# Optimization experiments

Measured on AMD Instinct MI355X. Metric: run time of the kernel, lower is better.

The kernel has to match this reference:

```python
import jax, jax.numpy as jnp
import numpy as np

B, N, L = 2, 2048, 2048
DQ, DKV, H, WF = 1024, 1024, 16, 4
HD = DQ // H
EPS = 1e-5


def _ln(x, g, b):
    m = jnp.mean(x, axis=-1, keepdims=True)
    v = jnp.mean(jnp.square(x - m), axis=-1, keepdims=True)
    return (x - m) * jax.lax.rsqrt(v + EPS) * g + b


def setup_inputs() -> dict:
    key = jax.random.key(0)
    ks = jax.random.split(key, 12)
    s = 0.02
    return {
        "x_q": jax.random.normal(ks[0], (B, N, DQ), jnp.float32),
        "x_kv": jax.random.normal(ks[1], (B, L, DKV), jnp.float32),
        "qn_g": jnp.ones((DQ,), jnp.float32),
        "qn_b": jnp.zeros((DQ,), jnp.float32),
        "kvn_g": jnp.ones((DKV,), jnp.float32),
        "kvn_b": jnp.zeros((DKV,), jnp.float32),
        "Wq": jax.random.normal(ks[2], (DQ, DQ), jnp.float32) * s,
        "bq": jnp.zeros((DQ,), jnp.float32),
        "Wk": jax.random.normal(ks[3], (DQ, DKV), jnp.float32) * s,
        "bk": jnp.zeros((DQ,), jnp.float32),
        "Wv": jax.random.normal(ks[4], (DQ, DKV), jnp.float32) * s,
        "bv": jnp.zeros((DQ,), jnp.float32),
        "Wo": jax.random.normal(ks[5], (DQ, DQ), jnp.float32) * s,
        "bo": jnp.zeros((DQ,), jnp.float32),
        "n2_g": jnp.ones((DQ,), jnp.float32),
        "n2_b": jnp.zeros((DQ,), jnp.float32),
        "W1": jax.random.normal(ks[6], (WF * DQ, DQ), jnp.float32) * s,
        "b1": jnp.zeros((WF * DQ,), jnp.float32),
        "W2": jax.random.normal(ks[7], (DQ, WF * DQ), jnp.float32) * s,
        "b2": jnp.zeros((DQ,), jnp.float32),
    }


def reference(x_q, x_kv, qn_g, qn_b, kvn_g, kvn_b, Wq, bq, Wk, bk, Wv, bv,
              Wo, bo, n2_g, n2_b, W1, b1, W2, b2):
    # projections (torch Linear: x @ W.T + b)
    q = (_ln(x_q, qn_g, qn_b) @ Wq.T + bq).reshape(B, N, H, HD)
    kvn = _ln(x_kv, kvn_g, kvn_b)
    k = (kvn @ Wk.T + bk).reshape(B, L, H, HD)
    v = (kvn @ Wv.T + bv).reshape(B, L, H, HD)

    # attention with softmax-1: exp(s)/(1 + sum exp(s)), numerically stable
    scale = 1.0 / jnp.sqrt(jnp.float32(HD))
    s = jnp.einsum("bnhd,blhd->bhnl", q, k) * scale  # [B,H,N,L]
    m = jnp.max(s, axis=-1, keepdims=True)
    m = jnp.maximum(m, 0.0)  # include the implicit zero logit of softmax-1
    p = jnp.exp(s - m)
    denom = jnp.sum(p, axis=-1, keepdims=True) + jnp.exp(-m)
    attn = p / denom
    attn_out = jnp.einsum("bhnl,blhd->bnhd", attn, v).reshape(B, N, DQ)

    # residual + out proj
    x = x_q + (attn_out @ Wo.T + bo)
    # residual MLP (GELU, exact/erf as torch nn.GELU default)
    h = jax.nn.gelu(_ln(x, n2_g, n2_b) @ W1.T + b1, approximate=False)
    x = x + (h @ W2.T + b2)
    return x
```

## Files before the change

### kernel.cpp

```cpp
#include <hip/hip_runtime.h>
#include <hip/hip_bf16.h>
#include <stdint.h>

#define DEV __device__ __forceinline__

typedef unsigned short ushort_t;
typedef __attribute__((ext_vector_type(8))) short bf16x8;
typedef __attribute__((ext_vector_type(4))) float f32x4;

DEV uint32_t f2bf2(float lo, float hi) {
  uint32_t d;
  asm("v_cvt_pk_bf16_f32 %0, %1, %2" : "=v"(d) : "v"(lo), "v"(hi));
  return d;
}
DEV ushort_t f2bf(float f) { return (ushort_t)f2bf2(f, f); }

DEV void gload_lds16(const void* gp, void* lp) {
  __builtin_amdgcn_global_load_lds(
      (__attribute__((address_space(1))) void*)(void*)(uintptr_t)gp,
      (__attribute__((address_space(3))) void*)lp, 16, 0, 0);
}

DEV float gelu_fast(float x) {
  const float z = fabsf(x) * 0.70710678118654752f;
  const float t = __builtin_amdgcn_rcpf(fmaf(0.3275911f, z, 1.0f));
  float p = fmaf(1.061405429f, t, -1.453152027f);
  p = fmaf(p, t, 1.421413741f);
  p = fmaf(p, t, -0.284496736f);
  p = fmaf(p, t, 0.254829592f);
  p *= t;
  const float e = __builtin_amdgcn_exp2f(z * z * -1.4426950408889634f);
  const float er = fmaf(-p, e, 1.0f);
  const float s = copysignf(er, x);
  return 0.5f * x * (1.0f + s);
}

DEV void ln_row(const float* __restrict__ x, const float* __restrict__ g,
                const float* __restrict__ be, ushort_t* __restrict__ out, int row) {
  const int t = threadIdx.x;
  const float4 v = ((const float4*)(x + (size_t)row * 1024))[t];
  float s = v.x + v.y + v.z + v.w;
  float sq = v.x * v.x + v.y * v.y + v.z * v.z + v.w * v.w;
#pragma unroll
  for (int d = 1; d < 64; d <<= 1) { s += __shfl_xor(s, d); sq += __shfl_xor(sq, d); }
  __shared__ float sm[8];
  const int w = t >> 6, lane = t & 63;
  if (lane == 0) { sm[w * 2] = s; sm[w * 2 + 1] = sq; }
  __syncthreads();
  s = sm[0] + sm[2] + sm[4] + sm[6];
  sq = sm[1] + sm[3] + sm[5] + sm[7];
  const float mean = s * (1.f / 1024.f);
  const float var = sq * (1.f / 1024.f) - mean * mean;
  const float rstd = rsqrtf(var + 1e-5f);
  const float4 gv = ((const float4*)g)[t];
  const float4 bv = ((const float4*)be)[t];
  uint2 o;
  o.x = f2bf2((v.x - mean) * rstd * gv.x + bv.x, (v.y - mean) * rstd * gv.y + bv.y);
  o.y = f2bf2((v.z - mean) * rstd * gv.z + bv.z, (v.w - mean) * rstd * gv.w + bv.w);
  ((uint2*)(out + (size_t)row * 1024))[t] = o;
}

__global__ __launch_bounds__(256) void cvt_ln(
    const float* __restrict__ Wq, const float* __restrict__ Wk,
    const float* __restrict__ Wv, const float* __restrict__ Wo,
    const float* __restrict__ W1, const float* __restrict__ W2,
    ushort_t* __restrict__ WQKVB, ushort_t* __restrict__ WoB,
    ushort_t* __restrict__ W1B, ushort_t* __restrict__ W2B,
    const float* __restrict__ x_q, const float* __restrict__ x_kv,
    const float* __restrict__ qg, const float* __restrict__ qb,
    const float* __restrict__ kg, const float* __restrict__ kb,
    ushort_t* __restrict__ oq, ushort_t* __restrict__ okv) {
  if (blockIdx.x < 12288) {
    int i = blockIdx.x * 256 + threadIdx.x;
    const float* src; ushort_t* dst; int j;
    if (i < 262144)            { src = Wq; dst = WQKVB;            j = i; }
    else if (i < 524288)       { src = Wk; dst = WQKVB + 1048576;  j = i - 262144; }
    else if (i < 786432)       { src = Wv; dst = WQKVB + 2097152;  j = i - 524288; }
    else if (i < 1048576)      { src = Wo; dst = WoB;              j = i - 786432; }
    else if (i < 2097152)      { src = W1; dst = W1B;              j = i - 1048576; }
    else                       { src = W2; dst = W2B;              j = i - 2097152; }
    float4 v = ((const float4*)src)[j];
    uint2 o; o.x = f2bf2(v.x, v.y); o.y = f2bf2(v.z, v.w);
    ((uint2*)dst)[j] = o;
  } else {
    const int r = blockIdx.x - 12288;
    if (r < 4096) ln_row(x_q, qg, qb, oq, r);
    else ln_row(x_kv, kg, kb, okv, r - 4096);
  }
}

__global__ __launch_bounds__(256) void ln_bf16(const float* __restrict__ x,
                                               const float* __restrict__ g,
                                               const float* __restrict__ be,
                                               ushort_t* __restrict__ out) {
  ln_row(x, g, be, out, blockIdx.x);
}

DEV void xcd_remap(int gx, int gy, int& bx, int& by) {
  const int lin = by * gx + bx;
  const int xcd = lin & 7, s = lin >> 3;
  by = xcd * (gy >> 3) + s / gx;
  bx = s % gx;
}

enum { EPI_BF16 = 0, EPI_KV = 1, EPI_RESID = 2, EPI_GELU = 3, EPI_QKV = 4 };

template <int BM, int TN, int BK, int EPI>
__global__ __launch_bounds__(256, (BM == 64) ? 4 : 3) void gemm_bt(
    const ushort_t* __restrict__ A,
    const ushort_t* __restrict__ A2,
    const ushort_t* __restrict__ Wb,
    const float* __restrict__ bias, const float* __restrict__ bias2,
    const float* __restrict__ bias3,
    const float* __restrict__ resid,
    void* __restrict__ outp, void* __restrict__ outp2, void* __restrict__ outp3,
    int M, int N, int K, float oscale) {
  constexpr int WAVES_N = (TN == 128 || BM == 64) ? 2 : 1;
  constexpr int WAVES_M = 4 / WAVES_N;
  constexpr int NI = BM / WAVES_M / 16;
  constexpr int NJ = TN / WAVES_N / 16;
  constexpr int CH = BK / 8;
  constexpr int NA = (BM * CH) / 256;
  constexpr int NBL = (TN * CH) / 256;
  constexpr int KS = BK / 32;
  __shared__ ushort_t As[2][BM * BK];
  __shared__ ushort_t Bs[2][TN * BK];
  const int t = threadIdx.x;
  const int w = t >> 6, lane = t & 63;
  const int qd = lane >> 4, ql = lane & 15;
  int bx = blockIdx.x, by = blockIdx.y;
  xcd_remap(gridDim.x, gridDim.y, bx, by);
  const int m0 = by * BM, n0 = bx * TN;
  const int wm = (w / WAVES_N) * (BM / WAVES_M);
  const int wn = (w % WAVES_N) * (TN / WAVES_N);
  const int sw = (BK == 64) ? (ql & 7) : ((ql >> 1) & 3);

  const ushort_t* Ause = (EPI == EPI_QKV && n0 >= 1024) ? A2 : A;

  const ushort_t* pa[NA];
#pragma unroll
  for (int p = 0; p < NA; p++) {
    int n = p * 256 + t, row = n / CH, c = n % CH;
    int g = (BK == 64) ? (c ^ (row & 7)) : (c ^ ((row >> 1) & 3));
    pa[p] = Ause + (size_t)(m0 + row) * K + g * 8;
  }
  const ushort_t* pb[NBL];
#pragma unroll
  for (int p = 0; p < NBL; p++) {
    int n = p * 256 + t, row = n / CH, c = n % CH;
    int g = (BK == 64) ? (c ^ (row & 7)) : (c ^ ((row >> 1) & 3));
    pb[p] = Wb + (size_t)(n0 + row) * K + g * 8;
  }

#pragma unroll
  for (int p = 0; p < NA; p++) { gload_lds16(pa[p], &As[0][(p * 256 + t) * 8]); pa[p] += BK; }
#pragma unroll
  for (int p = 0; p < NBL; p++) { gload_lds16(pb[p], &Bs[0][(p * 256 + t) * 8]); pb[p] += BK; }
  __syncthreads();

  f32x4 acc[NI][NJ] = {};
  const int NIT = K / BK;
  int cur = 0;

  for (int it = 0; it < NIT; ++it) {
    if (it + 1 < NIT) {
#pragma unroll
      for (int p = 0; p < NA; p++) { gload_lds16(pa[p], &As[1 ^ cur][(p * 256 + t) * 8]); pa[p] += BK; }
#pragma unroll
      for (int p = 0; p < NBL; p++) { gload_lds16(pb[p], &Bs[1 ^ cur][(p * 256 + t) * 8]); pb[p] += BK; }
    }
    const ushort_t* Ac = As[cur];
    const ushort_t* Bc = Bs[cur];
#pragma unroll
    for (int ks = 0; ks < KS; ks++) {
      bf16x8 af[NI], bf[NJ];
#pragma unroll
      for (int i = 0; i < NI; i++)
        af[i] = *(const bf16x8*)&Ac[(wm + i * 16 + ql) * BK + ((ks * 4 + qd) ^ sw) * 8];
#pragma unroll
      for (int j = 0; j < NJ; j++)
        bf[j] = *(const bf16x8*)&Bc[(wn + j * 16 + ql) * BK + ((ks * 4 + qd) ^ sw) * 8];
#pragma unroll
      for (int i = 0; i < NI; i++)
#pragma unroll
        for (int j = 0; j < NJ; j++)
          acc[i][j] = __builtin_amdgcn_mfma_f32_16x16x32_bf16(af[i], bf[j], acc[i][j], 0, 0, 0);
    }
    __syncthreads();
    cur ^= 1;
  }

#pragma unroll
  for (int i = 0; i < NI; i++) {
    const int mr = m0 + wm + i * 16 + qd * 4;
#pragma unroll
    for (int j = 0; j < NJ; j++) {
      const int col = n0 + wn + j * 16 + ql;
      f32x4 v = acc[i][j];
      if constexpr (EPI == EPI_BF16) {
        const float bb = bias[col];
        ushort_t* o = (ushort_t*)outp;
#pragma unroll
        for (int r = 0; r < 4; r++) o[(size_t)(mr + r) * N + col] = f2bf((v[r] + bb) * oscale);
      } else if constexpr (EPI == EPI_QKV) {
        if (col < 1024) {
          const float bb = bias[col];
          ushort_t* o = (ushort_t*)outp;
#pragma unroll
          for (int r = 0; r < 4; r++) o[(size_t)(mr + r) * 1024 + col] = f2bf((v[r] + bb) * oscale);
        } else if (col < 2048) {
          const int c2 = col - 1024;
          const float bb = bias2[c2];
          ushort_t* o = (ushort_t*)outp2;
#pragma unroll
          for (int r = 0; r < 4; r++) o[(size_t)(mr + r) * 1024 + c2] = f2bf(v[r] + bb);
        } else {
          const int vc = col - 2048;
          const float bb = bias3[vc];
          const int h = vc >> 6, d = vc & 63;
          const int b = mr >> 11, l0 = mr & 2047;
          uint2 pk;
          pk.x = f2bf2(v[0] + bb, v[1] + bb);
          pk.y = f2bf2(v[2] + bb, v[3] + bb);
          *(uint2*)((ushort_t*)outp3 + ((((size_t)b * 16 + h) * 64 + d) * 2048 + l0)) = pk;
        }
      } else if constexpr (EPI == EPI_RESID) {
        const float bb = bias[col];
        float* o = (float*)outp;
#pragma unroll
        for (int r = 0; r < 4; r++) {
          size_t idx = (size_t)(mr + r) * N + col;
          o[idx] = resid[idx] + v[r] + bb;
        }
      } else if constexpr (EPI == EPI_GELU) {
        const float bb = bias[col];
        ushort_t* o = (ushort_t*)outp;
#pragma unroll
        for (int r = 0; r < 4; r++)
          o[(size_t)(mr + r) * N + col] = f2bf(gelu_fast(v[r] + bb));
      }
    }
  }
}

template <int EPI>
__global__ __launch_bounds__(512, 2) void gemm256v2(
    const ushort_t* __restrict__ A, const ushort_t* __restrict__ Wb,
    const float* __restrict__ bias,
    void* __restrict__ outp, int M, int N, int K, float oscale) {
  __shared__ ushort_t As[2][256 * 64];
  __shared__ ushort_t Bs[2][256 * 64];
  const int t = threadIdx.x;
  const int w = t >> 6, lane = t & 63;
  const int qd = lane >> 4, ql = lane & 15;
  const int wr = w >> 2, wc = w & 3;
  int bx = blockIdx.x, by = blockIdx.y;
  xcd_remap(gridDim.x, gridDim.y, bx, by);
  const int m0 = by * 256, n0 = bx * 256;
  const int sw = ql & 7;

  const ushort_t* pa[4];
  const ushort_t* pb[4];
#pragma unroll
  for (int p = 0; p < 4; p++) {
    const int n = p * 512 + t, row = n >> 3, c = (n & 7) ^ (row & 7);
    pa[p] = A + (size_t)(m0 + row) * K + c * 8;
    pb[p] = Wb + (size_t)(n0 + row) * K + c * 8;
  }

#pragma unroll
  for (int p = 0; p < 4; p++) { gload_lds16(pa[p], &As[0][(p * 512 + t) * 8]); pa[p] += 64; }
#pragma unroll
  for (int p = 0; p < 4; p++) { gload_lds16(pb[p], &Bs[0][(p * 512 + t) * 8]); pb[p] += 64; }
  __syncthreads();

  f32x4 acc[8][4] = {};
  const int NT = K / 64;
  int cur = 0;

#define AFREAD(KS)                                                              \
  _Pragma("unroll") for (int i = 0; i < 8; i++)                                 \
      af[i] = *(const bf16x8*)&Ac[(wr * 128 + i * 16 + ql) * 64 +               \
                                  (((KS) * 4 + qd) ^ sw) * 8];
#define BFREAD(KS, NH)                                                          \
  _Pragma("unroll") for (int jj = 0; jj < 2; jj++)                              \
      bf[jj] = *(const bf16x8*)&Bc[(wc * 64 + (NH) * 32 + jj * 16 + ql) * 64 +  \
                                   (((KS) * 4 + qd) ^ sw) * 8];
#define MM(NH)                                                                  \
  __builtin_amdgcn_s_setprio(1);                                                \
  _Pragma("unroll") for (int i = 0; i < 8; i++)                                 \
      _Pragma("unroll") for (int jj = 0; jj < 2; jj++)                          \
          acc[i][(NH) * 2 + jj] = __builtin_amdgcn_mfma_f32_16x16x32_bf16(      \
              af[i], bf[jj], acc[i][(NH) * 2 + jj], 0, 0, 0);                   \
  __builtin_amdgcn_s_setprio(0);

  for (int T = 0; T < NT; ++T) {
    const ushort_t* Ac = As[cur];
    const ushort_t* Bc = Bs[cur];
    ushort_t* An = As[cur ^ 1];
    ushort_t* Bn = Bs[cur ^ 1];
    const bool st = (T + 1 < NT);
    bf16x8 af[8], bf[2];

    if (st) {
#pragma unroll
      for (int p = 0; p < 4; p++) { gload_lds16(pa[p], &An[(p * 512 + t) * 8]); pa[p] += 64; }
#pragma unroll
      for (int p = 0; p < 4; p++) { gload_lds16(pb[p], &Bn[(p * 512 + t) * 8]); pb[p] += 64; }
    }
    AFREAD(0)
    BFREAD(0, 0)
    MM(0)
    __builtin_amdgcn_s_barrier();

    BFREAD(0, 1)
    MM(1)
    __builtin_amdgcn_s_barrier();

    AFREAD(1)
    BFREAD(1, 0)
    MM(0)
    __builtin_amdgcn_s_barrier();

    BFREAD(1, 1)
    MM(1)
    if (st) asm volatile("s_waitcnt vmcnt(0)" ::: "memory");
    __builtin_amdgcn_sched_barrier(0);
    __builtin_amdgcn_s_barrier();
    __builtin_amdgcn_sched_barrier(0);
    cur ^= 1;
  }
#undef AFREAD
#undef BFREAD
#undef MM

#pragma unroll
  for (int i = 0; i < 8; i++) {
    const int mr = m0 + wr * 128 + i * 16 + qd * 4;
#pragma unroll
    for (int j = 0; j < 4; j++) {
      const int col = n0 + wc * 64 + j * 16 + ql;
      f32x4 v = acc[i][j];
      if constexpr (EPI == EPI_GELU) {
        const float bb = bias[col];
        ushort_t* o = (ushort_t*)outp;
#pragma unroll
        for (int r = 0; r < 4; r++)
          o[(size_t)(mr + r) * N + col] = f2bf(gelu_fast(v[r] + bb));
      } else if constexpr (EPI == EPI_BF16) {
        const float bb = bias[col];
        ushort_t* o = (ushort_t*)outp;
#pragma unroll
        for (int r = 0; r < 4; r++)
          o[(size_t)(mr + r) * N + col] = f2bf((v[r] + bb) * oscale);
      }
    }
  }
}

__global__ __launch_bounds__(256, 2) void flash_attn(const ushort_t* __restrict__ Qg,
                                                     const ushort_t* __restrict__ Kg,
                                                     const ushort_t* __restrict__ VTg,
                                                     ushort_t* __restrict__ Og) {
  __shared__ ushort_t QPs[128 * 64];
  __shared__ ushort_t Ks[2][64 * 64];
  __shared__ ushort_t Vs[2][64 * 64];
  const int t = threadIdx.x, w = t >> 6, lane = t & 63;
  const int qd = lane >> 4, ql = lane & 15;
  int bx = blockIdx.x, bh = blockIdx.y;
  xcd_remap(gridDim.x, gridDim.y, bx, bh);
  const int b = bh >> 4, h = bh & 15;
  const int n0 = bx * 128;
  const ushort_t* Qp = Qg + ((size_t)b * 2048 + n0) * 1024 + h * 64;
  const ushort_t* Kp = Kg + (size_t)b * 2048 * 1024 + h * 64;
  const ushort_t* Vp = VTg + (size_t)bh * 64 * 2048;
  const int sw = ql & 7;

  const ushort_t* kp2[2];
  const ushort_t* vp2[2];
#pragma unroll
  for (int p = 0; p < 2; p++) {
    int n = p * 256 + t, row = n >> 3, c = (n & 7) ^ (row & 7);
    kp2[p] = Kp + (size_t)row * 1024 + c * 8;
    vp2[p] = Vp + (size_t)row * 2048 + c * 8;
  }

#pragma unroll
  for (int p = 0; p < 4; p++) {
    int n = p * 256 + t, row = n >> 3, c = (n & 7) ^ (row & 7);
    gload_lds16(Qp + (size_t)row * 1024 + c * 8, &QPs[n * 8]);
  }
#pragma unroll
  for (int p = 0; p < 2; p++) { gload_lds16(kp2[p], &Ks[0][(p * 256 + t) * 8]); kp2[p] += 64 * 1024; }
  __syncthreads();

  bf16x8 aq[2][2];
#pragma unroll
  for (int i = 0; i < 2; i++)
#pragma unroll
    for (int ks = 0; ks < 2; ks++)
      aq[i][ks] = *(const bf16x8*)&QPs[(w * 32 + i * 16 + ql) * 64 + ((ks * 4 + qd) ^ sw) * 8];
  __syncthreads();

  f32x4 accA[4][2], accB[4][2];
  f32x4 accO[2][4] = {};
  float lro2[2] = {0.f, 0.f};
  const f32x4 ZZ = {0.f, 0.f, 0.f, 0.f};

#define QKSTEP(ACC, KSLOT)                                                                \
  { const ushort_t* Kc_ = &Ks[KSLOT][0];                                                  \
    bf16x8 bk[4];                                                                         \
    _Pragma("unroll") for (int j = 0; j < 4; j++)                                         \
      bk[j] = *(const bf16x8*)&Kc_[(j * 16 + ql) * 64 + ((0 + qd) ^ sw) * 8];             \
    __builtin_amdgcn_s_setprio(1);                                                        \
    _Pragma("unroll") for (int j = 0; j < 4; j++)                                         \
      _Pragma("unroll") for (int i = 0; i < 2; i++)                                       \
        ACC[j][i] = __builtin_amdgcn_mfma_f32_16x16x32_bf16(bk[j], aq[i][0], ZZ, 0, 0, 0);\
    __builtin_amdgcn_s_setprio(0);                                                        \
    _Pragma("unroll") for (int j = 0; j < 4; j++)                                         \
      bk[j] = *(const bf16x8*)&Kc_[(j * 16 + ql) * 64 + ((4 + qd) ^ sw) * 8];             \
    __builtin_amdgcn_s_setprio(1);                                                        \
    _Pragma("unroll") for (int j = 0; j < 4; j++)                                         \
      _Pragma("unroll") for (int i = 0; i < 2; i++)                                       \
        ACC[j][i] = __builtin_amdgcn_mfma_f32_16x16x32_bf16(bk[j], aq[i][1], ACC[j][i], 0, 0, 0); \
    __builtin_amdgcn_s_setprio(0);                                                        \
  }

#define SMSTEP(ACC)                                                                       \
  _Pragma("unroll") for (int j = 0; j < 4; j++)                                           \
    _Pragma("unroll") for (int i = 0; i < 2; i++) {                                       \
      f32x4 pp;                                                                           \
      _Pragma("unroll") for (int r = 0; r < 4; r++) {                                     \
        pp[r] = __builtin_amdgcn_exp2f(ACC[j][i][r]);                                     \
        lro2[i] += pp[r];                                                                 \
      }                                                                                   \
      const int nn = w * 32 + i * 16 + ql;                                                \
      const int coff = (((j * 2 + (qd >> 1)) ^ sw) << 3) + ((qd & 1) << 2);               \
      uint2 pk_; pk_.x = f2bf2(pp[0], pp[1]); pk_.y = f2bf2(pp[2], pp[3]);                \
      *(uint2*)&QPs[nn * 64 + coff] = pk_;                                                \
    }

#define PVSTEP(VSLOT)                                                                     \
  { const ushort_t* Vc_ = &Vs[VSLOT][0];                                                  \
    _Pragma("unroll") for (int ks = 0; ks < 2; ks++) {                                    \
      bf16x8 ap[2], bv[4];                                                                \
      _Pragma("unroll") for (int i = 0; i < 2; i++)                                       \
        ap[i] = *(const bf16x8*)&QPs[(w * 32 + i * 16 + ql) * 64 + ((ks * 4 + qd) ^ sw) * 8]; \
      _Pragma("unroll") for (int jo = 0; jo < 4; jo++)                                    \
        bv[jo] = *(const bf16x8*)&Vc_[(jo * 16 + ql) * 64 + ((ks * 4 + qd) ^ sw) * 8];    \
      __builtin_amdgcn_s_setprio(1);                                                      \
      _Pragma("unroll") for (int i = 0; i < 2; i++)                                       \
        _Pragma("unroll") for (int jo = 0; jo < 4; jo++)                                  \
          accO[i][jo] = __builtin_amdgcn_mfma_f32_16x16x32_bf16(ap[i], bv[jo], accO[i][jo], 0, 0, 0); \
      __builtin_amdgcn_s_setprio(0);                                                      \
    }                                                                                     \
  }

#define STAGE_K(SLOT)                                                                     \
  _Pragma("unroll") for (int q_ = 0; q_ < 2; q_++) {                                      \
    gload_lds16(kp2[q_], &Ks[SLOT][(q_ * 256 + t) * 8]); kp2[q_] += 64 * 1024;            \
  }
#define STAGE_V(SLOT)                                                                     \
  _Pragma("unroll") for (int q_ = 0; q_ < 2; q_++) {                                      \
    gload_lds16(vp2[q_], &Vs[SLOT][(q_ * 256 + t) * 8]); vp2[q_] += 64;                   \
  }

  STAGE_K(1)
  STAGE_V(0)
  QKSTEP(accA, 0)
  __syncthreads();

  for (int tt = 1; tt < 31; tt += 2) {
    STAGE_K(0)
    STAGE_V(1)
    QKSTEP(accB, 1)
    SMSTEP(accA)
    PVSTEP(0)
    __syncthreads();
    STAGE_K(1)
    STAGE_V(0)
    QKSTEP(accA, 0)
    SMSTEP(accB)
    PVSTEP(1)
    __syncthreads();
  }
  STAGE_V(1)
  QKSTEP(accB, 1)
  SMSTEP(accA)
  PVSTEP(0)
  __syncthreads();
  SMSTEP(accB)
  PVSTEP(1)

#undef QKSTEP
#undef SMSTEP
#undef PVSTEP
#undef STAGE_K
#undef STAGE_V

  float dn[2];
#pragma unroll
  for (int i = 0; i < 2; i++) {
    float l = lro2[i];
    l += __shfl_xor(l, 16);
    l += __shfl_xor(l, 32);
    dn[i] = l + 1.0f;
  }

#pragma unroll
  for (int i = 0; i < 2; i++)
#pragma unroll
    for (int r = 0; r < 4; r++) {
      const float inv = 1.0f / __shfl(dn[i], qd * 4 + r);
      const int row = n0 + w * 32 + i * 16 + qd * 4 + r;
#pragma unroll
      for (int jo = 0; jo < 4; jo++)
        Og[((size_t)b * 2048 + row) * 1024 + h * 64 + jo * 16 + ql] =
            f2bf(accO[i][jo][r] * inv);
    }
}

extern "C" void kernel_launch(void* const* d_in, const int* in_sizes, int n_in,
                              void* d_out, int out_size, void* d_ws, size_t ws_size,
                              hipStream_t stream) {
  const float* x_q = (const float*)d_in[0];
  const float* x_kv = (const float*)d_in[1];
  const float* qn_g = (const float*)d_in[2];
  const float* qn_b = (const float*)d_in[3];
  const float* kvn_g = (const float*)d_in[4];
  const float* kvn_b = (const float*)d_in[5];
  const float* Wq = (const float*)d_in[6];
  const float* bq = (const float*)d_in[7];
  const float* Wk = (const float*)d_in[8];
  const float* bk = (const float*)d_in[9];
  const float* Wv = (const float*)d_in[10];
  const float* bv = (const float*)d_in[11];
  const float* Wo = (const float*)d_in[12];
  const float* bo = (const float*)d_in[13];
  const float* n2_g = (const float*)d_in[14];
  const float* n2_b = (const float*)d_in[15];
  const float* W1 = (const float*)d_in[16];
  const float* b1 = (const float*)d_in[17];
  const float* W2 = (const float*)d_in[18];
  const float* b2 = (const float*)d_in[19];

  char* ws = (char*)d_ws;
  const size_t MB = 1ull << 20;
  ushort_t* WQKVB = (ushort_t*)(ws + 0 * MB);
  ushort_t* WoB = (ushort_t*)(ws + 6 * MB);
  ushort_t* W1B = (ushort_t*)(ws + 8 * MB);
  ushort_t* W2B = (ushort_t*)(ws + 16 * MB);
  ushort_t* LNQ = (ushort_t*)(ws + 24 * MB);
  ushort_t* LNKV = (ushort_t*)(ws + 32 * MB);
  ushort_t* Qb = (ushort_t*)(ws + 40 * MB);
  ushort_t* Kb = (ushort_t*)(ws + 48 * MB);
  ushort_t* VTb = (ushort_t*)(ws + 56 * MB);
  ushort_t* AOb = (ushort_t*)(ws + 64 * MB);
  float* Xf = (float*)(ws + 72 * MB);
  ushort_t* LN2 = (ushort_t*)(ws + 88 * MB);
  ushort_t* Hb = (ushort_t*)(ws + 24 * MB);

  const float QSCALE = 0.18033688011112042f;

  cvt_ln<<<20480, 256, 0, stream>>>(Wq, Wk, Wv, Wo, W1, W2, WQKVB, WoB, W1B, W2B,
                                    x_q, x_kv, qn_g, qn_b, kvn_g, kvn_b, LNQ, LNKV);

  gemm_bt<128, 128, 32, EPI_QKV><<<dim3(24, 32), 256, 0, stream>>>(
      LNQ, LNKV, WQKVB, bq, bk, bv, nullptr, Qb, Kb, VTb, 4096, 3072, 1024, QSCALE);

  flash_attn<<<dim3(16, 32), 256, 0, stream>>>(Qb, Kb, VTb, AOb);

  gemm_bt<64, 64, 64, EPI_RESID><<<dim3(16, 64), 256, 0, stream>>>(
      AOb, nullptr, WoB, bo, nullptr, nullptr, x_q, Xf, nullptr, nullptr,
      4096, 1024, 1024, 1.0f);
  ln_bf16<<<4096, 256, 0, stream>>>(Xf, n2_g, n2_b, LN2);
  gemm256v2<EPI_GELU><<<dim3(16, 16), 512, 0, stream>>>(
      LN2, W1B, b1, Hb, 4096, 4096, 1024, 1.0f);
  gemm_bt<64, 64, 64, EPI_RESID><<<dim3(16, 64), 256, 0, stream>>>(
      Hb, nullptr, W2B, b2, nullptr, nullptr, Xf, (float*)d_out, nullptr, nullptr,
      4096, 1024, 4096, 1.0f);
}
```

Measured before the change: 350.9 us.

## Overlap Wo/W1/W2 bf16 conversion with QKV GEMM via extra grid z-slice

Moves the fp32-to-bf16 conversion of Wo, W1 and W2 out of the initial cvt_ln kernel and into a second z-slice of the QKV GEMM launch. Those extra blocks only convert weights and return, so the memory-bound conversion can run alongside the compute-bound GEMM instead of before it. This shortens the serial prologue. The extra blocks compete with the GEMM for CUs and bandwidth, and the template now carries hardcoded grid constants (24, 196608).

After: 349.9 us. About the same (-0.3%).

```diff
diff --git a/kernel.cpp b/kernel.cpp
--- a/kernel.cpp
+++ b/kernel.cpp
@@ -62,28 +62,22 @@
 
 __global__ __launch_bounds__(256) void cvt_ln(
     const float* __restrict__ Wq, const float* __restrict__ Wk,
-    const float* __restrict__ Wv, const float* __restrict__ Wo,
-    const float* __restrict__ W1, const float* __restrict__ W2,
-    ushort_t* __restrict__ WQKVB, ushort_t* __restrict__ WoB,
-    ushort_t* __restrict__ W1B, ushort_t* __restrict__ W2B,
+    const float* __restrict__ Wv, ushort_t* __restrict__ WQKVB,
     const float* __restrict__ x_q, const float* __restrict__ x_kv,
     const float* __restrict__ qg, const float* __restrict__ qb,
     const float* __restrict__ kg, const float* __restrict__ kb,
     ushort_t* __restrict__ oq, ushort_t* __restrict__ okv) {
-  if (blockIdx.x < 12288) {
+  if (blockIdx.x < 3072) {
     int i = blockIdx.x * 256 + threadIdx.x;
-    const float* src; ushort_t* dst; int j;
-    if (i < 262144)            { src = Wq; dst = WQKVB;            j = i; }
-    else if (i < 524288)       { src = Wk; dst = WQKVB + 1048576;  j = i - 262144; }
-    else if (i < 786432)       { src = Wv; dst = WQKVB + 2097152;  j = i - 524288; }
-    else if (i < 1048576)      { src = Wo; dst = WoB;              j = i - 786432; }
-    else if (i < 2097152)      { src = W1; dst = W1B;              j = i - 1048576; }
-    else                       { src = W2; dst = W2B;              j = i - 2097152; }
+    const float* src; int j;
+    if (i < 262144)      { src = Wq; j = i; }
+    else if (i < 524288) { src = Wk; j = i - 262144; }
+    else                 { src = Wv; j = i - 524288; }
     float4 v = ((const float4*)src)[j];
     uint2 o; o.x = f2bf2(v.x, v.y); o.y = f2bf2(v.z, v.w);
-    ((uint2*)dst)[j] = o;
+    ((uint2*)WQKVB)[i] = o;
   } else {
-    const int r = blockIdx.x - 12288;
+    const int r = blockIdx.x - 3072;
     if (r < 4096) ln_row(x_q, qg, qb, oq, r);
     else ln_row(x_kv, kg, kb, okv, r - 4096);
   }
@@ -114,7 +108,27 @@
     const float* __restrict__ bias3,
     const float* __restrict__ resid,
     void* __restrict__ outp, void* __restrict__ outp2, void* __restrict__ outp3,
-    int M, int N, int K, float oscale) {
+    int M, int N, int K, float oscale,
+    const float* __restrict__ cWo = nullptr, const float* __restrict__ cW1 = nullptr,
+    const float* __restrict__ cW2 = nullptr, ushort_t* __restrict__ dWoB = nullptr,
+    ushort_t* __restrict__ dW1B = nullptr, ushort_t* __restrict__ dW2B = nullptr) {
+  if constexpr (EPI == EPI_QKV) {
+    if (blockIdx.z != 0) {
+      const int id0 = (blockIdx.y * 24 + blockIdx.x) * 256 + threadIdx.x;
+#pragma unroll
+      for (int it = 0; it < 12; it++) {
+        const int u = id0 + it * 196608;
+        const float* src; ushort_t* dst; int j;
+        if (u < 262144)       { src = cWo; dst = dWoB; j = u; }
+        else if (u < 1310720) { src = cW1; dst = dW1B; j = u - 262144; }
+        else                  { src = cW2; dst = dW2B; j = u - 1310720; }
+        float4 v = ((const float4*)src)[j];
+        uint2 o; o.x = f2bf2(v.x, v.y); o.y = f2bf2(v.z, v.w);
+        ((uint2*)dst)[j] = o;
+      }
+      return;
+    }
+  }
   constexpr int WAVES_N = (TN == 128 || BM == 64) ? 2 : 1;
   constexpr int WAVES_M = 4 / WAVES_N;
   constexpr int NI = BM / WAVES_M / 16;
@@ -562,11 +576,12 @@
 
   const float QSCALE = 0.18033688011112042f;
 
-  cvt_ln<<<20480, 256, 0, stream>>>(Wq, Wk, Wv, Wo, W1, W2, WQKVB, WoB, W1B, W2B,
+  cvt_ln<<<11264, 256, 0, stream>>>(Wq, Wk, Wv, WQKVB,
                                     x_q, x_kv, qn_g, qn_b, kvn_g, kvn_b, LNQ, LNKV);
 
-  gemm_bt<128, 128, 32, EPI_QKV><<<dim3(24, 32), 256, 0, stream>>>(
-      LNQ, LNKV, WQKVB, bq, bk, bv, nullptr, Qb, Kb, VTb, 4096, 3072, 1024, QSCALE);
+  gemm_bt<128, 128, 32, EPI_QKV><<<dim3(24, 32, 2), 256, 0, stream>>>(
+      LNQ, LNKV, WQKVB, bq, bk, bv, nullptr, Qb, Kb, VTb, 4096, 3072, 1024, QSCALE,
+      Wo, W1, W2, WoB, W1B, W2B);
 
   flash_attn<<<dim3(16, 32), 256, 0, stream>>>(Qb, Kb, VTb, AOb);
 
```
